# Performance work log

Hardware: AMD Instinct MI355X
Metric: run time of the kernel (lower is better)

## Reference

```python
import jax, jax.numpy as jnp
import numpy as np

NL, NK = 10000, 2000          # ligand / keypoint node counts
ELL, EKL = 320000, 160000     # lig->lig and kp->lig edge counts
IN, HID, OUT = 128, 128, 128  # in_size, hidden_size, out_size
FDIM = 2 * IN + 1             # edge MLP input: [h_src, h_dst, dij]


def silu(x):
    return x * jax.nn.sigmoid(x)


def setup_inputs() -> dict:
    keys = iter(jax.random.split(jax.random.key(0), 64))

    def nrm(shape, scale=0.02):
        return jax.random.normal(next(keys), shape, dtype=jnp.float32) * scale

    d = {}
    d["h_lig"] = jax.random.normal(next(keys), (NL, IN), dtype=jnp.float32)
    d["h_kp"] = jax.random.normal(next(keys), (NK, IN), dtype=jnp.float32)
    d["x_lig"] = jax.random.normal(next(keys), (NL, 3), dtype=jnp.float32)
    d["x_kp"] = jax.random.normal(next(keys), (NK, 3), dtype=jnp.float32)
    # per-node normalizer (e.g. neighbor count); keep >= 1 to avoid blowup
    d["z_lig"] = jax.random.uniform(next(keys), (NL, 1), dtype=jnp.float32, minval=1.0, maxval=32.0)
    for e in ("ll", "kl"):
        d[e + "_eW1"] = nrm((FDIM, HID)); d[e + "_eb1"] = jnp.zeros((HID,), jnp.float32)
        d[e + "_eW2"] = nrm((HID, HID)); d[e + "_eb2"] = jnp.zeros((HID,), jnp.float32)
        d[e + "_aW"] = nrm((HID, 1)); d[e + "_ab"] = jnp.zeros((1,), jnp.float32)
        d[e + "_cW1"] = nrm((FDIM, HID)); d[e + "_cb1"] = jnp.zeros((HID,), jnp.float32)
        d[e + "_cW2"] = nrm((HID, HID)); d[e + "_cb2"] = jnp.zeros((HID,), jnp.float32)
        d[e + "_cW3"] = nrm((HID, 1), scale=0.001)  # xavier gain=0.001 final coord layer
    d["n_W1"] = nrm((IN + HID, HID)); d["n_b1"] = jnp.zeros((HID,), jnp.float32)
    d["n_W2"] = nrm((HID, OUT)); d["n_b2"] = jnp.zeros((OUT,), jnp.float32)
    d["ll_src"] = jax.random.randint(next(keys), (ELL,), 0, NL, dtype=jnp.int32)
    d["ll_dst"] = jax.random.randint(next(keys), (ELL,), 0, NL, dtype=jnp.int32)
    d["kl_src"] = jax.random.randint(next(keys), (EKL,), 0, NK, dtype=jnp.int32)
    d["kl_dst"] = jax.random.randint(next(keys), (EKL,), 0, NL, dtype=jnp.int32)
    return d


def _edge_messages(hs, hd, xs, xd, eW1, eb1, eW2, eb2, aW, ab, cW1, cb1, cW2, cb2, cW3):
    x_diff = xs - xd                                     # fn.u_sub_v
    dij = jnp.linalg.norm(x_diff, axis=1, keepdims=True)  # [E,1]
    x_diff = x_diff / (dij + 1.0)
    f = jnp.concatenate([hs, hd, dij], axis=1)           # [E, 2*IN+1]
    m = silu(f @ eW1 + eb1)
    m = silu(m @ eW2 + eb2)
    msg_h = m * jax.nn.sigmoid(m @ aW + ab)              # soft attention gate
    c = silu(f @ cW1 + cb1)
    c = silu(c @ cW2 + cb2)
    msg_x = (c @ cW3) * x_diff                           # use_tanh=False path
    return msg_h, msg_x


def reference(h_lig, h_kp, x_lig, x_kp, z_lig,
              ll_eW1, ll_eb1, ll_eW2, ll_eb2, ll_aW, ll_ab,
              ll_cW1, ll_cb1, ll_cW2, ll_cb2, ll_cW3,
              kl_eW1, kl_eb1, kl_eW2, kl_eb2, kl_aW, kl_ab,
              kl_cW1, kl_cb1, kl_cW2, kl_cb2, kl_cW3,
              n_W1, n_b1, n_W2, n_b2,
              ll_src, ll_dst, kl_src, kl_dst):
    # lig -> lig edges
    mh_ll, mx_ll = _edge_messages(h_lig[ll_src], h_lig[ll_dst], x_lig[ll_src], x_lig[ll_dst],
                                  ll_eW1, ll_eb1, ll_eW2, ll_eb2, ll_aW, ll_ab,
                                  ll_cW1, ll_cb1, ll_cW2, ll_cb2, ll_cW3)
    # kp -> lig edges
    mh_kl, mx_kl = _edge_messages(h_kp[kl_src], h_lig[kl_dst], x_kp[kl_src], x_lig[kl_dst],
                                  kl_eW1, kl_eb1, kl_eW2, kl_eb2, kl_aW, kl_ab,
                                  kl_cW1, kl_cb1, kl_cW2, kl_cb2, kl_cW3)
    nl = h_lig.shape[0]
    # multi_update_all with cross_reducer='sum', then per-node normalization by z
    h_neigh = (jax.ops.segment_sum(mh_ll, ll_dst, num_segments=nl)
               + jax.ops.segment_sum(mh_kl, kl_dst, num_segments=nl)) / z_lig
    x_neigh = (jax.ops.segment_sum(mx_ll, ll_dst, num_segments=nl)
               + jax.ops.segment_sum(mx_kl, kl_dst, num_segments=nl)) / z_lig
    nin = jnp.concatenate([h_lig, h_neigh], axis=1)
    h_out = h_lig + (silu(nin @ n_W1 + n_b1) @ n_W2 + n_b2)  # norm=False -> Identity
    x_out = x_lig + x_neigh
    return (h_out, x_out)
```

## Files before the change

### kernel.cpp

```cpp
#include <hip/hip_runtime.h>
#include <hip/hip_bf16.h>
#include <math.h>

#define EPB  32
#define MSTR 136
#define FSTR 264

typedef __attribute__((ext_vector_type(8))) short short8;
typedef __attribute__((ext_vector_type(4))) float f32x4;

__device__ __forceinline__ unsigned short f2bf(float x) {
    unsigned int u = __float_as_uint(x);
    u += 0x7fffu + ((u >> 16) & 1u);
    return (unsigned short)(u >> 16);
}
__device__ __forceinline__ float bf2f(short v) {
    return __uint_as_float(((unsigned int)(unsigned short)v) << 16);
}
__device__ __forceinline__ unsigned int pkbf(float a, float b) {
    __hip_bfloat162 h = __float22bfloat162_rn(make_float2(a, b));
    union { __hip_bfloat162 h2; unsigned int u; } cv; cv.h2 = h; return cv.u;
}
__device__ __forceinline__ float frcp(float x) { return __builtin_amdgcn_rcpf(x); }
__device__ __forceinline__ float fsilu(float x) {
    return x * frcp(1.0f + __expf(-x));
}
__device__ __forceinline__ float fsigm(float x) {
    return frcp(1.0f + __expf(-x));
}
__device__ __forceinline__ void atomAddF(float* p, float v) {
    unsafeAtomicAdd(p, v);
}

template<int CTRL>
__device__ __forceinline__ float dppAdd(float x) {
    int y = __builtin_amdgcn_update_dpp(0, __float_as_int(x), CTRL, 0xF, 0xF, false);
    return x + __int_as_float(y);
}
__device__ __forceinline__ float rowSum16(float g) {
    g = dppAdd<0xB1>(g);
    g = dppAdd<0x4E>(g);
    g = dppAdd<0x124>(g);
    g = dppAdd<0x128>(g);
    return g;
}

struct PrepArgs { const float* src[10]; };

__global__ __launch_bounds__(256) void prep_hist_kernel(PrepArgs pa, short* __restrict__ wsb,
                                                        const int* __restrict__ lld,
                                                        const int* __restrict__ kld,
                                                        int* __restrict__ hist,
                                                        float* __restrict__ zfill) {
    int idx = blockIdx.x * 256 + threadIdx.x;
    if (idx < 245760) {
        int pair = idx / 49152;
        int rem  = idx - pair * 49152;
        int second = (rem >= 32768) ? 1 : 0;
        int mi = pair * 2 + second;
        int within = second ? (rem - 32768) : rem;
        int n, k, K;
        if (second) { K = 128; n = within >> 7; k = within & 127; }
        else        { K = 256; n = within >> 8; k = within & 255; }
        int dstoff = pair * 49152 + second * 32768;
        wsb[dstoff + n * K + k] = (short)f2bf(pa.src[mi][k * 128 + n]);
        return;
    }
    idx -= 245760;
    if (idx < 320000) { atomicAdd(&hist[lld[idx]], 1); return; }
    idx -= 320000;
    if (idx < 160000) { atomicAdd(&hist[10000 + kld[idx]], 1); return; }
    idx -= 160000;
    if (idx < 327500)
        ((float4*)zfill)[idx] = make_float4(0.f, 0.f, 0.f, 0.f);
}

struct ProjPair { const float* A; const short* Bt0; const short* Bt1; short* out;
                  const float* b0; const float* b1; int rows; int ktb; int hasb; };
struct BArgs {
    const int* hist;
    int* cursor;
    ProjPair p[4];
};

__global__ __launch_bounds__(256) void scan_proj_kernel(BArgs ba) {
    __shared__ __align__(16) short a_lds[64 * MSTR];
    const int t = threadIdx.x;
    if (blockIdx.x < 2) {
        __shared__ int ps[256];
        const int* h = ba.hist + blockIdx.x * 10000;
        int* cur = ba.cursor + blockIdx.x * 10000;
        const int base = t * 40;
        int v[40];
#pragma unroll
        for (int i = 0; i < 40; i++) {
            int ii = base + i;
            v[i] = (ii < 10000) ? h[ii] : 0;
        }
        int s = 0;
#pragma unroll
        for (int i = 0; i < 40; i++) s += v[i];
        ps[t] = s;
        __syncthreads();
        for (int off = 1; off < 256; off <<= 1) {
            int x = (t >= off) ? ps[t - off] : 0;
            __syncthreads();
            ps[t] += x;
            __syncthreads();
        }
        int run = ps[t] - s;
#pragma unroll
        for (int i = 0; i < 40; i++) {
            int ii = base + i;
            if (ii < 10000) { cur[ii] = run; run += v[i]; }
        }
        return;
    }
    const int pb = blockIdx.x - 2;
    const int pi = pb / 157, tile = pb - pi * 157;
    const ProjPair pd = ba.p[pi];
    if (tile * 64 >= pd.rows) return;
    {
        const int r = t >> 2, q = t & 3;
        const int node = tile * 64 + r;
        short* arow = a_lds + r * MSTR + q * 32;
        if (node < pd.rows) {
            const float* ap = pd.A + (size_t)node * 128 + q * 32;
#pragma unroll
            for (int i = 0; i < 4; i++) {
                float4 v0 = *(const float4*)(ap + i * 8);
                float4 v1 = *(const float4*)(ap + i * 8 + 4);
                uint4 o;
                o.x = pkbf(v0.x, v0.y); o.y = pkbf(v0.z, v0.w);
                o.z = pkbf(v1.x, v1.y); o.w = pkbf(v1.z, v1.w);
                *(uint4*)(arow + i * 8) = o;
            }
        } else {
            uint4 z = make_uint4(0, 0, 0, 0);
#pragma unroll
            for (int i = 0; i < 4; i++) *(uint4*)(arow + i * 8) = z;
        }
    }
    __syncthreads();

    const int ln = t & 63, wv = t >> 6;
    const int lrow = ln & 15, quad = ln >> 4;
    const int c0 = wv * 32 + lrow, c1 = c0 + 16;

#pragma unroll
    for (int g = 0; g < 2; g++) {
        const short* Bt = g ? pd.Bt1 : pd.Bt0;
        const float* bias = g ? pd.b1 : pd.b0;
        const int co = g * 128;
        short8 bf0[4], bf1[4];
#pragma unroll
        for (int kt = 0; kt < 4; kt++) {
            bf0[kt] = *(const short8*)(Bt + c0 * 256 + (pd.ktb + kt) * 32 + quad * 8);
            bf1[kt] = *(const short8*)(Bt + c1 * 256 + (pd.ktb + kt) * 32 + quad * 8);
        }
        const float bb0 = pd.hasb ? bias[c0] : 0.0f;
        const float bb1 = pd.hasb ? bias[c1] : 0.0f;
#pragma unroll
        for (int mt = 0; mt < 4; mt++) {
            short8 af[4];
#pragma unroll
            for (int kt = 0; kt < 4; kt++)
                af[kt] = *(const short8*)(&a_lds[(mt * 16 + lrow) * MSTR + kt * 32 + quad * 8]);
            f32x4 a0 = {0.f, 0.f, 0.f, 0.f}, a1 = {0.f, 0.f, 0.f, 0.f};
#pragma unroll
            for (int kt = 0; kt < 4; kt++) {
                a0 = __builtin_amdgcn_mfma_f32_16x16x32_bf16(af[kt], bf0[kt], a0, 0, 0, 0);
                a1 = __builtin_amdgcn_mfma_f32_16x16x32_bf16(af[kt], bf1[kt], a1, 0, 0, 0);
            }
#pragma unroll
            for (int r = 0; r < 4; r++) {
                const int node = tile * 64 + mt * 16 + quad * 4 + r;
                if (node < pd.rows) {
                    pd.out[(size_t)node * 256 + co + c0] = (short)f2bf(a0[r] + bb0);
                    pd.out[(size_t)node * 256 + co + c1] = (short)f2bf(a1[r] + bb1);
                }
            }
        }
    }
}

struct SArgs {
    const int *lls, *lld, *kls, *kld;
    int* cursor;
    int2 *ll_spk, *kl_spk;
};

__global__ __launch_bounds__(256) void scatter_kernel(SArgs sa) {
    int i = blockIdx.x * 256 + threadIdx.x;
    if (i < 320000) {
        int s = sa.lls[i];
        int d = sa.lld[i];
        int p = atomicAdd(&sa.cursor[d], 1);
        sa.ll_spk[p] = make_int2(s, d);
    } else if (i < 480000) {
        int j = i - 320000;
        int s = sa.kls[j];
        int d = sa.kld[j];
        int p = atomicAdd(&sa.cursor[10000 + d], 1);
        sa.kl_spk[p] = make_int2(s, d);
    }
}

struct EdgeSet {
    const short *Ps, *Pd;
    const float *xs, *xd;
    const int2 *esd;
    const float *w256e, *w256c;
    const short *W2t, *cW2t;
    const float *b2e, *b2c;
    const float *aW, *ab, *cW3;
};
struct EdgePair { EdgeSet s[2]; int split; };

__global__ __launch_bounds__(256, 6) void edge_kernel(EdgePair ep,
                                                      float* __restrict__ hne,
                                                      float* __restrict__ xne)
{
    __shared__ __align__(16) char mbuf[EPB * MSTR * 4];
    __shared__ float sv_l[EPB];
    __shared__ float gate_l[EPB];
    __shared__ float xdf[3][EPB];
    __shared__ int   dstl[EPB];
    __shared__ float gpc[4][EPB];
    __shared__ float gpe[4][EPB];

    short* mh = (short*)mbuf;
    short* mc = (short*)(mbuf + EPB * MSTR * 2);
    float* msg = (float*)mbuf;

    const int isKL = (blockIdx.x >= ep.split) ? 1 : 0;
    const EdgeSet P = ep.s[isKL];
    int b = blockIdx.x - (isKL ? ep.split : 0);
    const int nb8 = isKL ? 625 : 1250;
    b = (b & 7) * nb8 + (b >> 3);
    const int eb = b * EPB;
    const int t = threadIdx.x;

    {
        const int e = t >> 3, q = t & 7;
        const int eid = eb + e;
        const int2 sd = P.esd[eid];
        const int s = sd.x, d = sd.y;
        const short* psrow = P.Ps + (size_t)s * 256 + q * 16;
        const short* pdrow = P.Pd + (size_t)d * 256 + q * 16;
        short8 ra[2][2], rb[2][2];
#pragma unroll
        for (int path = 0; path < 2; path++)
#pragma unroll
            for (int i = 0; i < 2; i++) {
                ra[path][i] = *(const short8*)(psrow + path * 128 + i * 8);
                rb[path][i] = *(const short8*)(pdrow + path * 128 + i * 8);
            }
        float dx = P.xs[s * 3 + 0] - P.xd[d * 3 + 0];
        float dy = P.xs[s * 3 + 1] - P.xd[d * 3 + 1];
        float dz = P.xs[s * 3 + 2] - P.xd[d * 3 + 2];
        float dd = __builtin_amdgcn_sqrtf(dx * dx + dy * dy + dz * dz);
        if (q == 0) {
            dstl[e] = d;
            float inv = frcp(dd + 1.0f);
            xdf[0][e] = dx * inv; xdf[1][e] = dy * inv; xdf[2][e] = dz * inv;
        }
#pragma unroll
        for (int path = 0; path < 2; path++) {
            const float* wq = (path ? P.w256c : P.w256e) + q * 16;
            short* mrow = (path ? mc : mh) + e * MSTR + q * 16;
#pragma unroll
            for (int i = 0; i < 2; i++) {
                short8 a = ra[path][i];
                short8 b2 = rb[path][i];
                float4 wA = *(const float4*)(wq + i * 8);
                float4 wB = *(const float4*)(wq + i * 8 + 4);
                float v0 = fsilu(bf2f(a[0]) + bf2f(b2[0]) + dd * wA.x);
                float v1 = fsilu(bf2f(a[1]) + bf2f(b2[1]) + dd * wA.y);
                float v2 = fsilu(bf2f(a[2]) + bf2f(b2[2]) + dd * wA.z);
                float v3 = fsilu(bf2f(a[3]) + bf2f(b2[3]) + dd * wA.w);
                float v4 = fsilu(bf2f(a[4]) + bf2f(b2[4]) + dd * wB.x);
                float v5 = fsilu(bf2f(a[5]) + bf2f(b2[5]) + dd * wB.y);
                float v6 = fsilu(bf2f(a[6]) + bf2f(b2[6]) + dd * wB.z);
                float v7 = fsilu(bf2f(a[7]) + bf2f(b2[7]) + dd * wB.w);
                uint4 o;
                o.x = pkbf(v0, v1); o.y = pkbf(v2, v3);
                o.z = pkbf(v4, v5); o.w = pkbf(v6, v7);
                *(uint4*)(mrow + i * 8) = o;
            }
        }
    }
    __syncthreads();

    const int ln = t & 63, wv = t >> 6;
    const int lrow = ln & 15, quad = ln >> 4;
    const int c0 = wv * 32 + lrow, c1 = c0 + 16;

    {
        short8 bf0[4], bf1[4];
#pragma unroll
        for (int kt = 0; kt < 4; kt++) {
            bf0[kt] = *(const short8*)(P.cW2t + c0 * 128 + kt * 32 + quad * 8);
            bf1[kt] = *(const short8*)(P.cW2t + c1 * 128 + kt * 32 + quad * 8);
        }
        const float cw0 = P.cW3[c0], cw1 = P.cW3[c1];
        const float bb0 = P.b2c[c0], bb1 = P.b2c[c1];
#pragma unroll
        for (int mt = 0; mt < 2; mt++) {
            short8 af[4];
#pragma unroll
            for (int kt = 0; kt < 4; kt++)
                af[kt] = *(const short8*)(&mc[(mt * 16 + lrow) * MSTR + kt * 32 + quad * 8]);
            f32x4 a0 = {0.f, 0.f, 0.f, 0.f}, a1 = {0.f, 0.f, 0.f, 0.f};
#pragma unroll
            for (int kt = 0; kt < 4; kt++) {
                a0 = __builtin_amdgcn_mfma_f32_16x16x32_bf16(af[kt], bf0[kt], a0, 0, 0, 0);
                a1 = __builtin_amdgcn_mfma_f32_16x16x32_bf16(af[kt], bf1[kt], a1, 0, 0, 0);
            }
#pragma unroll
            for (int r = 0; r < 4; r++) {
                float v0 = fsilu(a0[r] + bb0);
                float v1 = fsilu(a1[r] + bb1);
                float g = rowSum16(v0 * cw0 + v1 * cw1);
                if (lrow == 0) gpc[wv][mt * 16 + quad * 4 + r] = g;
            }
        }
    }

    float m2s[2][8];
    {
        short8 bf0[4], bf1[4];
#pragma unroll
        for (int kt = 0; kt < 4; kt++) {
            bf0[kt] = *(const short8*)(P.W2t + c0 * 128 + kt * 32 + quad * 8);
            bf1[kt] = *(const short8*)(P.W2t + c1 * 128 + kt * 32 + quad * 8);
        }
        const float aw0 = P.aW[c0], aw1 = P.aW[c1];
        const float bb0 = P.b2e[c0], bb1 = P.b2e[c1];
#pragma unroll
        for (int mt = 0; mt < 2; mt++) {
            short8 af[4];
#pragma unroll
            for (int kt = 0; kt < 4; kt++)
                af[kt] = *(const short8*)(&mh[(mt * 16 + lrow) * MSTR + kt * 32 + quad * 8]);
            f32x4 a0 = {0.f, 0.f, 0.f, 0.f}, a1 = {0.f, 0.f, 0.f, 0.f};
#pragma unroll
            for (int kt = 0; kt < 4; kt++) {
                a0 = __builtin_amdgcn_mfma_f32_16x16x32_bf16(af[kt], bf0[kt], a0, 0, 0, 0);
                a1 = __builtin_amdgcn_mfma_f32_16x16x32_bf16(af[kt], bf1[kt], a1, 0, 0, 0);
            }
#pragma unroll
            for (int r = 0; r < 4; r++) {
                float v0 = fsilu(a0[r] + bb0);
                float v1 = fsilu(a1[r] + bb1);
                m2s[mt][r] = v0; m2s[mt][4 + r] = v1;
                float g = rowSum16(v0 * aw0 + v1 * aw1);
                if (lrow == 0) gpe[wv][mt * 16 + quad * 4 + r] = g;
            }
        }
    }
    __syncthreads();

    if (t < EPB) {
        sv_l[t]   = gpc[0][t] + gpc[1][t] + gpc[2][t] + gpc[3][t];
        gate_l[t] = fsigm(gpe[0][t] + gpe[1][t] + gpe[2][t] + gpe[3][t] + P.ab[0]);
    }
#pragma unroll
    for (int mt = 0; mt < 2; mt++)
#pragma unroll
        for (int r = 0; r < 4; r++) {
            const int erow = mt * 16 + quad * 4 + r;
            msg[erow * 132 + c0] = m2s[mt][r];
            msg[erow * 132 + c1] = m2s[mt][4 + r];
        }
    __syncthreads();

    {
        const int col = t & 127;
        const int e0 = (t >> 7) * 16;
        float acc = 0.0f;
        int cur = dstl[e0];
#pragma unroll 4
        for (int e = e0; e < e0 + 16; e++) {
            const int d = dstl[e];
            if (d != cur) {
                atomAddF(&hne[(size_t)cur * 128 + col], acc);
                acc = 0.0f; cur = d;
            }
            acc += msg[e * 132 + col] * gate_l[e];
        }
        atomAddF(&hne[(size_t)cur * 128 + col], acc);
    }
    if (t < 6) {
        const int ax = (t >= 3) ? (t - 3) : t;
        const int e0 = (t >= 3) ? 16 : 0;
        float acc = 0.0f;
        int cur = dstl[e0];
        for (int e = e0; e < e0 + 16; e++) {
            const int d = dstl[e];
            if (d != cur) {
                atomAddF(&xne[cur * 3 + ax], acc);
                acc = 0.0f; cur = d;
            }
            acc += sv_l[e] * xdf[ax][e];
        }
        atomAddF(&xne[cur * 3 + ax], acc);
    }
}

__global__ __launch_bounds__(256) void node_kernel(
    const float* __restrict__ h_lig, const float* __restrict__ zlig,
    const short* __restrict__ W1t, const float* __restrict__ b1v,
    const short* __restrict__ W2t, const float* __restrict__ b2v,
    const float* __restrict__ x_lig,
    const float* __restrict__ acc_h, const float* __restrict__ acc_x,
    float* __restrict__ h_out, float* __restrict__ x_out)
{
    __shared__ __align__(16) short f_lds[64 * FSTR];
    __shared__ __align__(16) short m_lds[64 * MSTR];
    const int t = threadIdx.x;
    const int nb = blockIdx.x * 64;

    {
        const int e = t >> 2, q = t & 3;
        const int node = nb + e;
        short* frow = &f_lds[e * FSTR + q * 32];
        if (node < 10000) {
            const float zi = frcp(zlig[node]);
            const float4* hp = (const float4*)(h_lig + (size_t)node * 128 + q * 32);
            const float4* np = (const float4*)(acc_h + (size_t)node * 128 + q * 32);
#pragma unroll
            for (int i = 0; i < 8; i++) {
                float4 v = hp[i];
                *(uint2*)(frow + i * 4) = make_uint2(pkbf(v.x, v.y), pkbf(v.z, v.w));
            }
#pragma unroll
            for (int i = 0; i < 8; i++) {
                float4 v = np[i];
                *(uint2*)(frow + 128 + i * 4) =
                    make_uint2(pkbf(v.x * zi, v.y * zi), pkbf(v.z * zi, v.w * zi));
            }
        } else {
            const uint2 zz = make_uint2(0, 0);
#pragma unroll
            for (int i = 0; i < 8; i++) {
                *(uint2*)(frow + i * 4) = zz;
                *(uint2*)(frow + 128 + i * 4) = zz;
            }
        }
    }
    __syncthreads();

    const int ln = t & 63, wv = t >> 6;
    const int lrow = ln & 15, quad = ln >> 4;
    const int c0 = wv * 32 + lrow, c1 = c0 + 16;

    {
        short8 bf0[8], bf1[8];
#pragma unroll
        for (int kt = 0; kt < 8; kt++) {
            bf0[kt] = *(const short8*)(W1t + c0 * 256 + kt * 32 + quad * 8);
            bf1[kt] = *(const short8*)(W1t + c1 * 256 + kt * 32 + quad * 8);
        }
        const float bb0 = b1v[c0], bb1 = b1v[c1];
#pragma unroll
        for (int mt = 0; mt < 4; mt++) {
            short8 af[8];
#pragma unroll
            for (int kt = 0; kt < 8; kt++)
                af[kt] = *(const short8*)(&f_lds[(mt * 16 + lrow) * FSTR + kt * 32 + quad * 8]);
            f32x4 a0 = {0.f, 0.f, 0.f, 0.f}, a1 = {0.f, 0.f, 0.f, 0.f};
#pragma unroll
            for (int kt = 0; kt < 8; kt++) {
                a0 = __builtin_amdgcn_mfma_f32_16x16x32_bf16(af[kt], bf0[kt], a0, 0, 0, 0);
                a1 = __builtin_amdgcn_mfma_f32_16x16x32_bf16(af[kt], bf1[kt], a1, 0, 0, 0);
            }
#pragma unroll
            for (int r = 0; r < 4; r++) {
                const int erow = mt * 16 + quad * 4 + r;
                m_lds[erow * MSTR + c0] = (short)f2bf(fsilu(a0[r] + bb0));
                m_lds[erow * MSTR + c1] = (short)f2bf(fsilu(a1[r] + bb1));
            }
        }
    }
    __syncthreads();

    {
        short8 bf0[4], bf1[4];
#pragma unroll
        for (int kt = 0; kt < 4; kt++) {
            bf0[kt] = *(const short8*)(W2t + c0 * 128 + kt * 32 + quad * 8);
            bf1[kt] = *(const short8*)(W2t + c1 * 128 + kt * 32 + quad * 8);
        }
        const float bb0 = b2v[c0], bb1 = b2v[c1];
#pragma unroll
        for (int mt = 0; mt < 4; mt++) {
            short8 af[4];
#pragma unroll
            for (int kt = 0; kt < 4; kt++)
                af[kt] = *(const short8*)(&m_lds[(mt * 16 + lrow) * MSTR + kt * 32 + quad * 8]);
            f32x4 a0 = {0.f, 0.f, 0.f, 0.f}, a1 = {0.f, 0.f, 0.f, 0.f};
#pragma unroll
            for (int kt = 0; kt < 4; kt++) {
                a0 = __builtin_amdgcn_mfma_f32_16x16x32_bf16(af[kt], bf0[kt], a0, 0, 0, 0);
                a1 = __builtin_amdgcn_mfma_f32_16x16x32_bf16(af[kt], bf1[kt], a1, 0, 0, 0);
            }
#pragma unroll
            for (int r = 0; r < 4; r++) {
                const int node = nb + mt * 16 + quad * 4 + r;
                if (node < 10000) {
                    h_out[(size_t)node * 128 + c0] = a0[r] + bb0 + h_lig[(size_t)node * 128 + c0];
                    h_out[(size_t)node * 128 + c1] = a1[r] + bb1 + h_lig[(size_t)node * 128 + c1];
                }
            }
        }
    }
    if (t < 64) {
        const int node = nb + t;
        if (node < 10000) {
            const float zi = frcp(zlig[node]);
#pragma unroll
            for (int i = 0; i < 3; i++)
                x_out[node * 3 + i] = x_lig[node * 3 + i] + acc_x[node * 3 + i] * zi;
        }
    }
}

extern "C" void kernel_launch(void* const* d_in, const int* in_sizes, int n_in,
                              void* d_out, int out_size, void* d_ws, size_t ws_size,
                              hipStream_t stream)
{
    (void)in_sizes; (void)n_in; (void)ws_size; (void)out_size;
    const float* h_lig  = (const float*)d_in[0];
    const float* h_kp   = (const float*)d_in[1];
    const float* x_lig  = (const float*)d_in[2];
    const float* x_kp   = (const float*)d_in[3];
    const float* z_lig  = (const float*)d_in[4];
    const float* ll_eW1 = (const float*)d_in[5];
    const float* ll_eb1 = (const float*)d_in[6];
    const float* ll_eW2 = (const float*)d_in[7];
    const float* ll_eb2 = (const float*)d_in[8];
    const float* ll_aW  = (const float*)d_in[9];
    const float* ll_ab  = (const float*)d_in[10];
    const float* ll_cW1 = (const float*)d_in[11];
    const float* ll_cb1 = (const float*)d_in[12];
    const float* ll_cW2 = (const float*)d_in[13];
    const float* ll_cb2 = (const float*)d_in[14];
    const float* ll_cW3 = (const float*)d_in[15];
    const float* kl_eW1 = (const float*)d_in[16];
    const float* kl_eb1 = (const float*)d_in[17];
    const float* kl_eW2 = (const float*)d_in[18];
    const float* kl_eb2 = (const float*)d_in[19];
    const float* kl_aW  = (const float*)d_in[20];
    const float* kl_ab  = (const float*)d_in[21];
    const float* kl_cW1 = (const float*)d_in[22];
    const float* kl_cb1 = (const float*)d_in[23];
    const float* kl_cW2 = (const float*)d_in[24];
    const float* kl_cb2 = (const float*)d_in[25];
    const float* kl_cW3 = (const float*)d_in[26];
    const float* n_W1   = (const float*)d_in[27];
    const float* n_b1   = (const float*)d_in[28];
    const float* n_W2   = (const float*)d_in[29];
    const float* n_b2   = (const float*)d_in[30];
    const int* ll_src = (const int*)d_in[31];
    const int* ll_dst = (const int*)d_in[32];
    const int* kl_src = (const int*)d_in[33];
    const int* kl_dst = (const int*)d_in[34];

    float* h_out = (float*)d_out;
    float* x_out = h_out + 1280000;

    char* wsc = (char*)d_ws;
    short* wsb    = (short*)wsc;
    short* P_ll_s = (short*)(wsc +   491520);
    short* P_ll_d = (short*)(wsc +  5611520);
    short* P_kl_s = (short*)(wsc + 10731520);
    short* P_kl_d = (short*)(wsc + 11755520);
    int2* ll_spk  = (int2*)(wsc + 16875520);
    int2* kl_spk  = (int2*)(wsc + 19435520);
    int* hist     = (int*)(wsc + 20715520);
    int* cursor   = (int*)(wsc + 20795520);
    float* hne    = (float*)(wsc + 20875520);
    float* xne    = (float*)(wsc + 25995520);

    (void)hipMemsetAsync(hist, 0, 80000, stream);

    {
        PrepArgs pa;
        pa.src[0] = ll_eW1; pa.src[1] = ll_eW2; pa.src[2] = ll_cW1; pa.src[3] = ll_cW2;
        pa.src[4] = kl_eW1; pa.src[5] = kl_eW2; pa.src[6] = kl_cW1; pa.src[7] = kl_cW2;
        pa.src[8] = n_W1;   pa.src[9] = n_W2;
        prep_hist_kernel<<<4115, 256, 0, stream>>>(pa, wsb, ll_dst, kl_dst, hist, hne);
    }
    {
        BArgs ba;
        ba.hist = hist; ba.cursor = cursor;
        ba.p[0] = { h_lig, wsb + 0,     wsb + 49152,  P_ll_s, ll_eb1, ll_cb1, 10000, 0, 0 };
        ba.p[1] = { h_lig, wsb + 0,     wsb + 49152,  P_ll_d, ll_eb1, ll_cb1, 10000, 4, 1 };
        ba.p[2] = { h_kp,  wsb + 98304, wsb + 147456, P_kl_s, kl_eb1, kl_cb1,  2000, 0, 0 };
        ba.p[3] = { h_lig, wsb + 98304, wsb + 147456, P_kl_d, kl_eb1, kl_cb1, 10000, 4, 1 };
        scan_proj_kernel<<<2 + 4 * 157, 256, 0, stream>>>(ba);
    }
    {
        SArgs sa;
        sa.lls = ll_src; sa.lld = ll_dst; sa.kls = kl_src; sa.kld = kl_dst;
        sa.cursor = cursor;
        sa.ll_spk = ll_spk; sa.kl_spk = kl_spk;
        scatter_kernel<<<1875, 256, 0, stream>>>(sa);
    }
    {
        EdgePair ep;
        ep.split = 10000;
        ep.s[0] = { P_ll_s, P_ll_d, x_lig, x_lig, ll_spk,
                    ll_eW1 + 256 * 128, ll_cW1 + 256 * 128,
                    wsb + 32768, wsb + 81920, ll_eb2, ll_cb2,
                    ll_aW, ll_ab, ll_cW3 };
        ep.s[1] = { P_kl_s, P_kl_d, x_kp, x_lig, kl_spk,
                    kl_eW1 + 256 * 128, kl_cW1 + 256 * 128,
                    wsb + 131072, wsb + 180224, kl_eb2, kl_cb2,
                    kl_aW, kl_ab, kl_cW3 };
        edge_kernel<<<15000, 256, 0, stream>>>(ep, hne, xne);
    }
    node_kernel<<<157, 256, 0, stream>>>(
        h_lig, z_lig, wsb + 196608, n_b1, wsb + 229376, n_b2,
        x_lig, hne, xne, h_out, x_out);
}
```

Measured before the change: 371.0 us.

## Process four edge tiles per block with double-buffered gather prefetch; fuse scatter with projection

The edge kernel now handles four 32-edge tiles per block. It prefetches the next tile's gathered projections into registers and double-buffers the LDS message tiles, so gather latency overlaps the MFMA work of the current tile. The grid shrinks from 15000 to 3750 blocks, and occupancy drops from 6 to 4 blocks per CU because LDS use roughly doubles. Separately, the scan is split into its own tiny kernel and the scatter is fused into the projection kernel. The weight-transpose loop in prep is also reindexed so its reads are coalesced.

Measured after the change: 400.1 us. 1.08x slower.

```diff
diff --git a/kernel.cpp b/kernel.cpp
--- a/kernel.cpp
+++ b/kernel.cpp
@@ -2,9 +2,10 @@
 #include <hip/hip_bf16.h>
 #include <math.h>
 
-#define EPB  32
-#define MSTR 136
-#define FSTR 264
+#define EPB   32
+#define TEDGE 4
+#define MSTR  136
+#define FSTR  264
 
 typedef __attribute__((ext_vector_type(8))) short short8;
 typedef __attribute__((ext_vector_type(4))) float f32x4;
@@ -59,9 +60,9 @@
         int second = (rem >= 32768) ? 1 : 0;
         int mi = pair * 2 + second;
         int within = second ? (rem - 32768) : rem;
-        int n, k, K;
-        if (second) { K = 128; n = within >> 7; k = within & 127; }
-        else        { K = 256; n = within >> 8; k = within & 255; }
+        int K = second ? 128 : 256;
+        int n = within & 127;
+        int k = within >> 7;
         int dstoff = pair * 49152 + second * 32768;
         wsb[dstoff + n * K + k] = (short)f2bf(pa.src[mi][k * 128 + n]);
         return;
@@ -75,50 +76,69 @@
         ((float4*)zfill)[idx] = make_float4(0.f, 0.f, 0.f, 0.f);
 }
 
+__global__ __launch_bounds__(256) void scan_kernel(const int* __restrict__ hist,
+                                                   int* __restrict__ cursor) {
+    __shared__ int ps[256];
+    const int t = threadIdx.x;
+    const int* h = hist + blockIdx.x * 10000;
+    int* cur = cursor + blockIdx.x * 10000;
+    const int base = t * 40;
+    int v[40];
+#pragma unroll
+    for (int i = 0; i < 40; i++) {
+        int ii = base + i;
+        v[i] = (ii < 10000) ? h[ii] : 0;
+    }
+    int s = 0;
+#pragma unroll
+    for (int i = 0; i < 40; i++) s += v[i];
+    ps[t] = s;
+    __syncthreads();
+    for (int off = 1; off < 256; off <<= 1) {
+        int x = (t >= off) ? ps[t - off] : 0;
+        __syncthreads();
+        ps[t] += x;
+        __syncthreads();
+    }
+    int run = ps[t] - s;
+#pragma unroll
+    for (int i = 0; i < 40; i++) {
+        int ii = base + i;
+        if (ii < 10000) { cur[ii] = run; run += v[i]; }
+    }
+}
+
 struct ProjPair { const float* A; const short* Bt0; const short* Bt1; short* out;
                   const float* b0; const float* b1; int rows; int ktb; int hasb; };
-struct BArgs {
-    const int* hist;
+struct CArgs {
+    const int *lls, *lld, *kls, *kld;
     int* cursor;
+    int2 *ll_spk, *kl_spk;
     ProjPair p[4];
 };
 
-__global__ __launch_bounds__(256) void scan_proj_kernel(BArgs ba) {
+__global__ __launch_bounds__(256) void scatter_proj_kernel(CArgs ca) {
     __shared__ __align__(16) short a_lds[64 * MSTR];
     const int t = threadIdx.x;
-    if (blockIdx.x < 2) {
-        __shared__ int ps[256];
-        const int* h = ba.hist + blockIdx.x * 10000;
-        int* cur = ba.cursor + blockIdx.x * 10000;
-        const int base = t * 40;
-        int v[40];
-#pragma unroll
-        for (int i = 0; i < 40; i++) {
-            int ii = base + i;
-            v[i] = (ii < 10000) ? h[ii] : 0;
-        }
-        int s = 0;
-#pragma unroll
-        for (int i = 0; i < 40; i++) s += v[i];
-        ps[t] = s;
-        __syncthreads();
-        for (int off = 1; off < 256; off <<= 1) {
-            int x = (t >= off) ? ps[t - off] : 0;
-            __syncthreads();
-            ps[t] += x;
-            __syncthreads();
-        }
-        int run = ps[t] - s;
-#pragma unroll
-        for (int i = 0; i < 40; i++) {
-            int ii = base + i;
-            if (ii < 10000) { cur[ii] = run; run += v[i]; }
+    if (blockIdx.x < 1875) {
+        int i = blockIdx.x * 256 + t;
+        if (i < 320000) {
+            int s = ca.lls[i];
+            int d = ca.lld[i];
+            int p = atomicAdd(&ca.cursor[d], 1);
+            ca.ll_spk[p] = make_int2(s, d);
+        } else if (i < 480000) {
+            int j = i - 320000;
+            int s = ca.kls[j];
+            int d = ca.kld[j];
+            int p = atomicAdd(&ca.cursor[10000 + d], 1);
+            ca.kl_spk[p] = make_int2(s, d);
         }
         return;
     }
-    const int pb = blockIdx.x - 2;
+    const int pb = blockIdx.x - 1875;
     const int pi = pb / 157, tile = pb - pi * 157;
-    const ProjPair pd = ba.p[pi];
+    const ProjPair pd = ca.p[pi];
     if (tile * 64 >= pd.rows) return;
     {
         const int r = t >> 2, q = t & 3;
@@ -181,28 +201,6 @@
                 }
             }
         }
-    }
-}
-
-struct SArgs {
-    const int *lls, *lld, *kls, *kld;
-    int* cursor;
-    int2 *ll_spk, *kl_spk;
-};
-
-__global__ __launch_bounds__(256) void scatter_kernel(SArgs sa) {
-    int i = blockIdx.x * 256 + threadIdx.x;
-    if (i < 320000) {
-        int s = sa.lls[i];
-        int d = sa.lld[i];
-        int p = atomicAdd(&sa.cursor[d], 1);
-        sa.ll_spk[p] = make_int2(s, d);
-    } else if (i < 480000) {
-        int j = i - 320000;
-        int s = sa.kls[j];
-        int d = sa.kld[j];
-        int p = atomicAdd(&sa.cursor[10000 + d], 1);
-        sa.kl_spk[p] = make_int2(s, d);
     }
 }
 
@@ -215,40 +213,53 @@
     const float *b2e, *b2c;
     const float *aW, *ab, *cW3;
 };
-struct EdgePair { EdgeSet s[2]; int split; };
-
-__global__ __launch_bounds__(256, 6) void edge_kernel(EdgePair ep,
+struct EdgePair { EdgeSet s[2]; };
+
+__global__ __launch_bounds__(256, 4) void edge_kernel(EdgePair ep,
                                                       float* __restrict__ hne,
                                                       float* __restrict__ xne)
 {
-    __shared__ __align__(16) char mbuf[EPB * MSTR * 4];
+    __shared__ __align__(16) char mbuf[2][EPB * MSTR * 4];
     __shared__ float sv_l[EPB];
     __shared__ float gate_l[EPB];
-    __shared__ float xdf[3][EPB];
-    __shared__ int   dstl[EPB];
+    __shared__ float xdf[2][3][EPB];
+    __shared__ int   dstl[2][EPB];
     __shared__ float gpc[4][EPB];
     __shared__ float gpe[4][EPB];
 
-    short* mh = (short*)mbuf;
-    short* mc = (short*)(mbuf + EPB * MSTR * 2);
-    float* msg = (float*)mbuf;
-
-    const int isKL = (blockIdx.x >= ep.split) ? 1 : 0;
+    const int isKL = (blockIdx.x >= 2500) ? 1 : 0;
     const EdgeSet P = ep.s[isKL];
-    int b = blockIdx.x - (isKL ? ep.split : 0);
-    const int nb8 = isKL ? 625 : 1250;
-    b = (b & 7) * nb8 + (b >> 3);
-    const int eb = b * EPB;
+    int b = blockIdx.x - (isKL ? 2500 : 0);
+    {
+        const int nb = isKL ? 1250 : 2500;
+        const int q8 = nb >> 3, r8 = nb & 7;
+        const int xcd = b & 7, bi = b >> 3;
+        b = (xcd < r8 ? xcd * (q8 + 1) : r8 * (q8 + 1) + (xcd - r8) * q8) + bi;
+    }
+    const int tile0 = b * TEDGE;
     const int t = threadIdx.x;
-
-    {
-        const int e = t >> 3, q = t & 7;
-        const int eid = eb + e;
+    const int e = t >> 3, q = t & 7;
+    const int ln = t & 63, wv = t >> 6;
+    const int lrow = ln & 15, quad = ln >> 4;
+    const int c0 = wv * 32 + lrow, c1 = c0 + 16;
+
+    const float cw3_0 = P.cW3[c0], cw3_1 = P.cW3[c1];
+    const float b2c_0 = P.b2c[c0], b2c_1 = P.b2c[c1];
+    const float aw_0  = P.aW[c0],  aw_1  = P.aW[c1];
+    const float b2e_0 = P.b2e[c0], b2e_1 = P.b2e[c1];
+    const float ab0   = P.ab[0];
+
+    short8 ra[2][2], rb[2][2];
+    float sdx, sdy, sdz, sdd;
+    int   sd_d;
+
+    auto STAGE = [&](int g) {
+        const int eid = g * EPB + e;
         const int2 sd = P.esd[eid];
         const int s = sd.x, d = sd.y;
+        sd_d = d;
         const short* psrow = P.Ps + (size_t)s * 256 + q * 16;
         const short* pdrow = P.Pd + (size_t)d * 256 + q * 16;
-        short8 ra[2][2], rb[2][2];
 #pragma unroll
         for (int path = 0; path < 2; path++)
 #pragma unroll
@@ -256,22 +267,28 @@
                 ra[path][i] = *(const short8*)(psrow + path * 128 + i * 8);
                 rb[path][i] = *(const short8*)(pdrow + path * 128 + i * 8);
             }
-        float dx = P.xs[s * 3 + 0] - P.xd[d * 3 + 0];
-        float dy = P.xs[s * 3 + 1] - P.xd[d * 3 + 1];
-        float dz = P.xs[s * 3 + 2] - P.xd[d * 3 + 2];
-        float dd = __builtin_amdgcn_sqrtf(dx * dx + dy * dy + dz * dz);
+        sdx = P.xs[s * 3 + 0] - P.xd[d * 3 + 0];
+        sdy = P.xs[s * 3 + 1] - P.xd[d * 3 + 1];
+        sdz = P.xs[s * 3 + 2] - P.xd[d * 3 + 2];
+        sdd = __builtin_amdgcn_sqrtf(sdx * sdx + sdy * sdy + sdz * sdz);
+    };
+
+    auto PACK = [&](int nx) {
+        short* mhw = (short*)mbuf[nx];
+        short* mcw = mhw + EPB * MSTR;
         if (q == 0) {
-            dstl[e] = d;
-            float inv = frcp(dd + 1.0f);
-            xdf[0][e] = dx * inv; xdf[1][e] = dy * inv; xdf[2][e] = dz * inv;
-        }
+            dstl[nx][e] = sd_d;
+            float inv = frcp(sdd + 1.0f);
+            xdf[nx][0][e] = sdx * inv; xdf[nx][1][e] = sdy * inv; xdf[nx][2][e] = sdz * inv;
+        }
+        const float dd = sdd;
 #pragma unroll
         for (int path = 0; path < 2; path++) {
             const float* wq = (path ? P.w256c : P.w256e) + q * 16;
-            short* mrow = (path ? mc : mh) + e * MSTR + q * 16;
+            short* mrow = (path ? mcw : mhw) + e * MSTR + q * 16;
 #pragma unroll
             for (int i = 0; i < 2; i++) {
-                short8 a = ra[path][i];
+                short8 a  = ra[path][i];
                 short8 b2 = rb[path][i];
                 float4 wA = *(const float4*)(wq + i * 8);
                 float4 wB = *(const float4*)(wq + i * 8 + 4);
@@ -289,122 +306,127 @@
                 *(uint4*)(mrow + i * 8) = o;
             }
         }
-    }
+    };
+
+    STAGE(tile0);
+    PACK(0);
     __syncthreads();
 
-    const int ln = t & 63, wv = t >> 6;
-    const int lrow = ln & 15, quad = ln >> 4;
-    const int c0 = wv * 32 + lrow, c1 = c0 + 16;
-
-    {
-        short8 bf0[4], bf1[4];
-#pragma unroll
-        for (int kt = 0; kt < 4; kt++) {
-            bf0[kt] = *(const short8*)(P.cW2t + c0 * 128 + kt * 32 + quad * 8);
-            bf1[kt] = *(const short8*)(P.cW2t + c1 * 128 + kt * 32 + quad * 8);
-        }
-        const float cw0 = P.cW3[c0], cw1 = P.cW3[c1];
-        const float bb0 = P.b2c[c0], bb1 = P.b2c[c1];
-#pragma unroll
-        for (int mt = 0; mt < 2; mt++) {
-            short8 af[4];
-#pragma unroll
-            for (int kt = 0; kt < 4; kt++)
-                af[kt] = *(const short8*)(&mc[(mt * 16 + lrow) * MSTR + kt * 32 + quad * 8]);
-            f32x4 a0 = {0.f, 0.f, 0.f, 0.f}, a1 = {0.f, 0.f, 0.f, 0.f};
+    for (int ti = 0; ti < TEDGE; ++ti) {
+        const int cur = ti & 1;
+        short* mh  = (short*)mbuf[cur];
+        short* mc  = mh + EPB * MSTR;
+        float* msg = (float*)mbuf[cur];
+
+        if (ti + 1 < TEDGE) STAGE(tile0 + ti + 1);
+
+        {
+            short8 bf0[4], bf1[4];
 #pragma unroll
             for (int kt = 0; kt < 4; kt++) {
-                a0 = __builtin_amdgcn_mfma_f32_16x16x32_bf16(af[kt], bf0[kt], a0, 0, 0, 0);
-                a1 = __builtin_amdgcn_mfma_f32_16x16x32_bf16(af[kt], bf1[kt], a1, 0, 0, 0);
-            }
+                bf0[kt] = *(const short8*)(P.cW2t + c0 * 128 + kt * 32 + quad * 8);
+                bf1[kt] = *(const short8*)(P.cW2t + c1 * 128 + kt * 32 + quad * 8);
+            }
+#pragma unroll
+            for (int mt = 0; mt < 2; mt++) {
+                short8 af[4];
+#pragma unroll
+                for (int kt = 0; kt < 4; kt++)
+                    af[kt] = *(const short8*)(&mc[(mt * 16 + lrow) * MSTR + kt * 32 + quad * 8]);
+                f32x4 a0 = {0.f, 0.f, 0.f, 0.f}, a1 = {0.f, 0.f, 0.f, 0.f};
+#pragma unroll
+                for (int kt = 0; kt < 4; kt++) {
+                    a0 = __builtin_amdgcn_mfma_f32_16x16x32_bf16(af[kt], bf0[kt], a0, 0, 0, 0);
+                    a1 = __builtin_amdgcn_mfma_f32_16x16x32_bf16(af[kt], bf1[kt], a1, 0, 0, 0);
+                }
+#pragma unroll
+                for (int r = 0; r < 4; r++) {
+                    float v0 = fsilu(a0[r] + b2c_0);
+                    float v1 = fsilu(a1[r] + b2c_1);
+                    float g = rowSum16(v0 * cw3_0 + v1 * cw3_1);
+                    if (lrow == 0) gpc[wv][mt * 16 + quad * 4 + r] = g;
+                }
+            }
+        }
+
+        float m2s[2][8];
+        {
+            short8 bf0[4], bf1[4];
+#pragma unroll
+            for (int kt = 0; kt < 4; kt++) {
+                bf0[kt] = *(const short8*)(P.W2t + c0 * 128 + kt * 32 + quad * 8);
+                bf1[kt] = *(const short8*)(P.W2t + c1 * 128 + kt * 32 + quad * 8);
+            }
+#pragma unroll
+            for (int mt = 0; mt < 2; mt++) {
+                short8 af[4];
+#pragma unroll
+                for (int kt = 0; kt < 4; kt++)
+                    af[kt] = *(const short8*)(&mh[(mt * 16 + lrow) * MSTR + kt * 32 + quad * 8]);
+                f32x4 a0 = {0.f, 0.f, 0.f, 0.f}, a1 = {0.f, 0.f, 0.f, 0.f};
+#pragma unroll
+                for (int kt = 0; kt < 4; kt++) {
+                    a0 = __builtin_amdgcn_mfma_f32_16x16x32_bf16(af[kt], bf0[kt], a0, 0, 0, 0);
+                    a1 = __builtin_amdgcn_mfma_f32_16x16x32_bf16(af[kt], bf1[kt], a1, 0, 0, 0);
+                }
+#pragma unroll
+                for (int r = 0; r < 4; r++) {
+                    float v0 = fsilu(a0[r] + b2e_0);
+                    float v1 = fsilu(a1[r] + b2e_1);
+                    m2s[mt][r] = v0; m2s[mt][4 + r] = v1;
+                    float g = rowSum16(v0 * aw_0 + v1 * aw_1);
+                    if (lrow == 0) gpe[wv][mt * 16 + quad * 4 + r] = g;
+                }
+            }
+        }
+        __syncthreads();
+
+        if (t < EPB) {
+            sv_l[t]   = gpc[0][t] + gpc[1][t] + gpc[2][t] + gpc[3][t];
+            gate_l[t] = fsigm(gpe[0][t] + gpe[1][t] + gpe[2][t] + gpe[3][t] + ab0);
+        }
+#pragma unroll
+        for (int mt = 0; mt < 2; mt++)
 #pragma unroll
             for (int r = 0; r < 4; r++) {
-                float v0 = fsilu(a0[r] + bb0);
-                float v1 = fsilu(a1[r] + bb1);
-                float g = rowSum16(v0 * cw0 + v1 * cw1);
-                if (lrow == 0) gpc[wv][mt * 16 + quad * 4 + r] = g;
-            }
-        }
-    }
-
-    float m2s[2][8];
-    {
-        short8 bf0[4], bf1[4];
-#pragma unroll
-        for (int kt = 0; kt < 4; kt++) {
-            bf0[kt] = *(const short8*)(P.W2t + c0 * 128 + kt * 32 + quad * 8);
-            bf1[kt] = *(const short8*)(P.W2t + c1 * 128 + kt * 32 + quad * 8);
-        }
-        const float aw0 = P.aW[c0], aw1 = P.aW[c1];
-        const float bb0 = P.b2e[c0], bb1 = P.b2e[c1];
-#pragma unroll
-        for (int mt = 0; mt < 2; mt++) {
-            short8 af[4];
-#pragma unroll
-            for (int kt = 0; kt < 4; kt++)
-                af[kt] = *(const short8*)(&mh[(mt * 16 + lrow) * MSTR + kt * 32 + quad * 8]);
-            f32x4 a0 = {0.f, 0.f, 0.f, 0.f}, a1 = {0.f, 0.f, 0.f, 0.f};
-#pragma unroll
-            for (int kt = 0; kt < 4; kt++) {
-                a0 = __builtin_amdgcn_mfma_f32_16x16x32_bf16(af[kt], bf0[kt], a0, 0, 0, 0);
-                a1 = __builtin_amdgcn_mfma_f32_16x16x32_bf16(af[kt], bf1[kt], a1, 0, 0, 0);
-            }
-#pragma unroll
-            for (int r = 0; r < 4; r++) {
-                float v0 = fsilu(a0[r] + bb0);
-                float v1 = fsilu(a1[r] + bb1);
-                m2s[mt][r] = v0; m2s[mt][4 + r] = v1;
-                float g = rowSum16(v0 * aw0 + v1 * aw1);
-                if (lrow == 0) gpe[wv][mt * 16 + quad * 4 + r] = g;
-            }
-        }
-    }
-    __syncthreads();
-
-    if (t < EPB) {
-        sv_l[t]   = gpc[0][t] + gpc[1][t] + gpc[2][t] + gpc[3][t];
-        gate_l[t] = fsigm(gpe[0][t] + gpe[1][t] + gpe[2][t] + gpe[3][t] + P.ab[0]);
-    }
-#pragma unroll
-    for (int mt = 0; mt < 2; mt++)
-#pragma unroll
-        for (int r = 0; r < 4; r++) {
-            const int erow = mt * 16 + quad * 4 + r;
-            msg[erow * 132 + c0] = m2s[mt][r];
-            msg[erow * 132 + c1] = m2s[mt][4 + r];
-        }
-    __syncthreads();
-
-    {
-        const int col = t & 127;
-        const int e0 = (t >> 7) * 16;
-        float acc = 0.0f;
-        int cur = dstl[e0];
+                const int erow = mt * 16 + quad * 4 + r;
+                msg[erow * 132 + c0] = m2s[mt][r];
+                msg[erow * 132 + c1] = m2s[mt][4 + r];
+            }
+        if (ti + 1 < TEDGE) PACK(cur ^ 1);
+        __syncthreads();
+
+        {
+            const int col = t & 127;
+            const int e0 = (t >> 7) * 16;
+            float acc = 0.0f;
+            int curd = dstl[cur][e0];
 #pragma unroll 4
-        for (int e = e0; e < e0 + 16; e++) {
-            const int d = dstl[e];
-            if (d != cur) {
-                atomAddF(&hne[(size_t)cur * 128 + col], acc);
-                acc = 0.0f; cur = d;
-            }
-            acc += msg[e * 132 + col] * gate_l[e];
-        }
-        atomAddF(&hne[(size_t)cur * 128 + col], acc);
-    }
-    if (t < 6) {
-        const int ax = (t >= 3) ? (t - 3) : t;
-        const int e0 = (t >= 3) ? 16 : 0;
-        float acc = 0.0f;
-        int cur = dstl[e0];
-        for (int e = e0; e < e0 + 16; e++) {
-            const int d = dstl[e];
-            if (d != cur) {
-                atomAddF(&xne[cur * 3 + ax], acc);
-                acc = 0.0f; cur = d;
-            }
-            acc += sv_l[e] * xdf[ax][e];
-        }
-        atomAddF(&xne[cur * 3 + ax], acc);
+            for (int ee = e0; ee < e0 + 16; ee++) {
+                const int d = dstl[cur][ee];
+                if (d != curd) {
+                    atomAddF(&hne[(size_t)curd * 128 + col], acc);
+                    acc = 0.0f; curd = d;
+                }
+                acc += msg[ee * 132 + col] * gate_l[ee];
+            }
+            atomAddF(&hne[(size_t)curd * 128 + col], acc);
+        }
+        if (t < 6) {
+            const int ax = (t >= 3) ? (t - 3) : t;
+            const int e0 = (t >= 3) ? 16 : 0;
+            float acc = 0.0f;
+            int curd = dstl[cur][e0];
+            for (int ee = e0; ee < e0 + 16; ee++) {
+                const int d = dstl[cur][ee];
+                if (d != curd) {
+                    atomAddF(&xne[curd * 3 + ax], acc);
+                    acc = 0.0f; curd = d;
+                }
+                acc += sv_l[ee] * xdf[cur][ax][ee];
+            }
+            atomAddF(&xne[curd * 3 + ax], acc);
+        }
     }
 }
 
@@ -592,25 +614,20 @@
         pa.src[8] = n_W1;   pa.src[9] = n_W2;
         prep_hist_kernel<<<4115, 256, 0, stream>>>(pa, wsb, ll_dst, kl_dst, hist, hne);
     }
-    {
-        BArgs ba;
-        ba.hist = hist; ba.cursor = cursor;
-        ba.p[0] = { h_lig, wsb + 0,     wsb + 49152,  P_ll_s, ll_eb1, ll_cb1, 10000, 0, 0 };
-        ba.p[1] = { h_lig, wsb + 0,     wsb + 49152,  P_ll_d, ll_eb1, ll_cb1, 10000, 4, 1 };
-        ba.p[2] = { h_kp,  wsb + 98304, wsb + 147456, P_kl_s, kl_eb1, kl_cb1,  2000, 0, 0 };
-        ba.p[3] = { h_lig, wsb + 98304, wsb + 147456, P_kl_d, kl_eb1, kl_cb1, 10000, 4, 1 };
-        scan_proj_kernel<<<2 + 4 * 157, 256, 0, stream>>>(ba);
-    }
-    {
-        SArgs sa;
-        sa.lls = ll_src; sa.lld = ll_dst; sa.kls = kl_src; sa.kld = kl_dst;
-        sa.cursor = cursor;
-        sa.ll_spk = ll_spk; sa.kl_spk = kl_spk;
-        scatter_kernel<<<1875, 256, 0, stream>>>(sa);
+    scan_kernel<<<2, 256, 0, stream>>>(hist, cursor);
+    {
+        CArgs ca;
+        ca.lls = ll_src; ca.lld = ll_dst; ca.kls = kl_src; ca.kld = kl_dst;
+        ca.cursor = cursor;
+        ca.ll_spk = ll_spk; ca.kl_spk = kl_spk;
+        ca.p[0] = { h_lig, wsb + 0,     wsb + 49152,  P_ll_s, ll_eb1, ll_cb1, 10000, 0, 0 };
+        ca.p[1] = { h_lig, wsb + 0,     wsb + 49152,  P_ll_d, ll_eb1, ll_cb1, 10000, 4, 1 };
+        ca.p[2] = { h_kp,  wsb + 98304, wsb + 147456, P_kl_s, kl_eb1, kl_cb1,  2000, 0, 0 };
+        ca.p[3] = { h_lig, wsb + 98304, wsb + 147456, P_kl_d, kl_eb1, kl_cb1, 10000, 4, 1 };
+        scatter_proj_kernel<<<1875 + 4 * 157, 256, 0, stream>>>(ca);
     }
     {
         EdgePair ep;
-        ep.split = 10000;
         ep.s[0] = { P_ll_s, P_ll_d, x_lig, x_lig, ll_spk,
                     ll_eW1 + 256 * 128, ll_cW1 + 256 * 128,
                     wsb + 32768, wsb + 81920, ll_eb2, ll_cb2,
@@ -619,7 +636,7 @@
                     kl_eW1 + 256 * 128, kl_cW1 + 256 * 128,
                     wsb + 131072, wsb + 180224, kl_eb2, kl_cb2,
                     kl_aW, kl_ab, kl_cW3 };
-        edge_kernel<<<15000, 256, 0, stream>>>(ep, hne, xne);
+        edge_kernel<<<3750, 256, 0, stream>>>(ep, hne, xne);
     }
     node_kernel<<<157, 256, 0, stream>>>(
         h_lig, z_lig, wsb + 196608, n_b1, wsb + 229376, n_b2,
```

## Fuse histogram into scan blocks via LDS bins and merge scatter with projection

Applied to the files above, without the earlier changes.

The dst-degree histogram moves from global atomics into two blocks that count bins in shared memory and then scan them, which removes the hipMemsetAsync and one kernel launch. The weight transpose indexing now makes consecutive threads read contiguous source elements. The edge scatter and the node projection GEMM now share one launch, so the projection no longer waits behind the scatter kernel. The cost is that two single blocks walk 320k and 160k indices serially, which may lengthen the critical path of the prep kernel.

After: 425.9 us. 14.8% more time.

```diff
diff --git a/kernel.cpp b/kernel.cpp
--- a/kernel.cpp
+++ b/kernel.cpp
@@ -47,55 +47,32 @@
 
 struct PrepArgs { const float* src[10]; };
 
-__global__ __launch_bounds__(256) void prep_hist_kernel(PrepArgs pa, short* __restrict__ wsb,
+__global__ __launch_bounds__(256) void prep_scan_kernel(PrepArgs pa, short* __restrict__ wsb,
                                                         const int* __restrict__ lld,
                                                         const int* __restrict__ kld,
-                                                        int* __restrict__ hist,
+                                                        int* __restrict__ cursor,
                                                         float* __restrict__ zfill) {
-    int idx = blockIdx.x * 256 + threadIdx.x;
-    if (idx < 245760) {
-        int pair = idx / 49152;
-        int rem  = idx - pair * 49152;
-        int second = (rem >= 32768) ? 1 : 0;
-        int mi = pair * 2 + second;
-        int within = second ? (rem - 32768) : rem;
-        int n, k, K;
-        if (second) { K = 128; n = within >> 7; k = within & 127; }
-        else        { K = 256; n = within >> 8; k = within & 255; }
-        int dstoff = pair * 49152 + second * 32768;
-        wsb[dstoff + n * K + k] = (short)f2bf(pa.src[mi][k * 128 + n]);
-        return;
-    }
-    idx -= 245760;
-    if (idx < 320000) { atomicAdd(&hist[lld[idx]], 1); return; }
-    idx -= 320000;
-    if (idx < 160000) { atomicAdd(&hist[10000 + kld[idx]], 1); return; }
-    idx -= 160000;
-    if (idx < 327500)
-        ((float4*)zfill)[idx] = make_float4(0.f, 0.f, 0.f, 0.f);
-}
-
-struct ProjPair { const float* A; const short* Bt0; const short* Bt1; short* out;
-                  const float* b0; const float* b1; int rows; int ktb; int hasb; };
-struct BArgs {
-    const int* hist;
-    int* cursor;
-    ProjPair p[4];
-};
-
-__global__ __launch_bounds__(256) void scan_proj_kernel(BArgs ba) {
-    __shared__ __align__(16) short a_lds[64 * MSTR];
+    __shared__ int bins[10000];
+    __shared__ int ps[256];
     const int t = threadIdx.x;
     if (blockIdx.x < 2) {
-        __shared__ int ps[256];
-        const int* h = ba.hist + blockIdx.x * 10000;
-        int* cur = ba.cursor + blockIdx.x * 10000;
+        const int n4 = blockIdx.x ? 40000 : 80000;
+        const int4* d4 = (const int4*)(blockIdx.x ? kld : lld);
+        int* cur = cursor + blockIdx.x * 10000;
+        for (int i = t; i < 10000; i += 256) bins[i] = 0;
+        __syncthreads();
+        for (int i = t; i < n4; i += 256) {
+            int4 v = d4[i];
+            atomicAdd(&bins[v.x], 1); atomicAdd(&bins[v.y], 1);
+            atomicAdd(&bins[v.z], 1); atomicAdd(&bins[v.w], 1);
+        }
+        __syncthreads();
         const int base = t * 40;
         int v[40];
 #pragma unroll
         for (int i = 0; i < 40; i++) {
             int ii = base + i;
-            v[i] = (ii < 10000) ? h[ii] : 0;
+            v[i] = (ii < 10000) ? bins[ii] : 0;
         }
         int s = 0;
 #pragma unroll
@@ -116,9 +93,56 @@
         }
         return;
     }
-    const int pb = blockIdx.x - 2;
+    int idx = (blockIdx.x - 2) * 256 + t;
+    if (idx < 245760) {
+        int pair = idx / 49152;
+        int rem  = idx - pair * 49152;
+        int second = (rem >= 32768) ? 1 : 0;
+        int mi = pair * 2 + second;
+        int within = second ? (rem - 32768) : rem;
+        int K = second ? 128 : 256;
+        int n = within & 127;
+        int k = within >> 7;
+        int dstoff = pair * 49152 + second * 32768;
+        wsb[dstoff + n * K + k] = (short)f2bf(pa.src[mi][k * 128 + n]);
+        return;
+    }
+    idx -= 245760;
+    if (idx < 327500)
+        ((float4*)zfill)[idx] = make_float4(0.f, 0.f, 0.f, 0.f);
+}
+
+struct ProjPair { const float* A; const short* Bt0; const short* Bt1; short* out;
+                  const float* b0; const float* b1; int rows; int ktb; int hasb; };
+struct CArgs {
+    const int *lls, *lld, *kls, *kld;
+    int* cursor;
+    int2 *ll_spk, *kl_spk;
+    ProjPair p[4];
+};
+
+__global__ __launch_bounds__(256) void scatter_proj_kernel(CArgs ca) {
+    __shared__ __align__(16) short a_lds[64 * MSTR];
+    const int t = threadIdx.x;
+    if (blockIdx.x < 1875) {
+        int i = blockIdx.x * 256 + t;
+        if (i < 320000) {
+            int s = ca.lls[i];
+            int d = ca.lld[i];
+            int p = atomicAdd(&ca.cursor[d], 1);
+            ca.ll_spk[p] = make_int2(s, d);
+        } else if (i < 480000) {
+            int j = i - 320000;
+            int s = ca.kls[j];
+            int d = ca.kld[j];
+            int p = atomicAdd(&ca.cursor[10000 + d], 1);
+            ca.kl_spk[p] = make_int2(s, d);
+        }
+        return;
+    }
+    const int pb = blockIdx.x - 1875;
     const int pi = pb / 157, tile = pb - pi * 157;
-    const ProjPair pd = ba.p[pi];
+    const ProjPair pd = ca.p[pi];
     if (tile * 64 >= pd.rows) return;
     {
         const int r = t >> 2, q = t & 3;
@@ -181,28 +205,6 @@
                 }
             }
         }
-    }
-}
-
-struct SArgs {
-    const int *lls, *lld, *kls, *kld;
-    int* cursor;
-    int2 *ll_spk, *kl_spk;
-};
-
-__global__ __launch_bounds__(256) void scatter_kernel(SArgs sa) {
-    int i = blockIdx.x * 256 + threadIdx.x;
-    if (i < 320000) {
-        int s = sa.lls[i];
-        int d = sa.lld[i];
-        int p = atomicAdd(&sa.cursor[d], 1);
-        sa.ll_spk[p] = make_int2(s, d);
-    } else if (i < 480000) {
-        int j = i - 320000;
-        int s = sa.kls[j];
-        int d = sa.kld[j];
-        int p = atomicAdd(&sa.cursor[10000 + d], 1);
-        sa.kl_spk[p] = make_int2(s, d);
     }
 }
 
@@ -578,35 +580,27 @@
     short* P_kl_d = (short*)(wsc + 11755520);
     int2* ll_spk  = (int2*)(wsc + 16875520);
     int2* kl_spk  = (int2*)(wsc + 19435520);
-    int* hist     = (int*)(wsc + 20715520);
     int* cursor   = (int*)(wsc + 20795520);
     float* hne    = (float*)(wsc + 20875520);
     float* xne    = (float*)(wsc + 25995520);
-
-    (void)hipMemsetAsync(hist, 0, 80000, stream);
 
     {
         PrepArgs pa;
         pa.src[0] = ll_eW1; pa.src[1] = ll_eW2; pa.src[2] = ll_cW1; pa.src[3] = ll_cW2;
         pa.src[4] = kl_eW1; pa.src[5] = kl_eW2; pa.src[6] = kl_cW1; pa.src[7] = kl_cW2;
         pa.src[8] = n_W1;   pa.src[9] = n_W2;
-        prep_hist_kernel<<<4115, 256, 0, stream>>>(pa, wsb, ll_dst, kl_dst, hist, hne);
-    }
-    {
-        BArgs ba;
-        ba.hist = hist; ba.cursor = cursor;
-        ba.p[0] = { h_lig, wsb + 0,     wsb + 49152,  P_ll_s, ll_eb1, ll_cb1, 10000, 0, 0 };
-        ba.p[1] = { h_lig, wsb + 0,     wsb + 49152,  P_ll_d, ll_eb1, ll_cb1, 10000, 4, 1 };
-        ba.p[2] = { h_kp,  wsb + 98304, wsb + 147456, P_kl_s, kl_eb1, kl_cb1,  2000, 0, 0 };
-        ba.p[3] = { h_lig, wsb + 98304, wsb + 147456, P_kl_d, kl_eb1, kl_cb1, 10000, 4, 1 };
-        scan_proj_kernel<<<2 + 4 * 157, 256, 0, stream>>>(ba);
-    }
-    {
-        SArgs sa;
-        sa.lls = ll_src; sa.lld = ll_dst; sa.kls = kl_src; sa.kld = kl_dst;
-        sa.cursor = cursor;
-        sa.ll_spk = ll_spk; sa.kl_spk = kl_spk;
-        scatter_kernel<<<1875, 256, 0, stream>>>(sa);
+        prep_scan_kernel<<<2242, 256, 0, stream>>>(pa, wsb, ll_dst, kl_dst, cursor, hne);
+    }
+    {
+        CArgs ca;
+        ca.lls = ll_src; ca.lld = ll_dst; ca.kls = kl_src; ca.kld = kl_dst;
+        ca.cursor = cursor;
+        ca.ll_spk = ll_spk; ca.kl_spk = kl_spk;
+        ca.p[0] = { h_lig, wsb + 0,     wsb + 49152,  P_ll_s, ll_eb1, ll_cb1, 10000, 0, 0 };
+        ca.p[1] = { h_lig, wsb + 0,     wsb + 49152,  P_ll_d, ll_eb1, ll_cb1, 10000, 4, 1 };
+        ca.p[2] = { h_kp,  wsb + 98304, wsb + 147456, P_kl_s, kl_eb1, kl_cb1,  2000, 0, 0 };
+        ca.p[3] = { h_lig, wsb + 98304, wsb + 147456, P_kl_d, kl_eb1, kl_cb1, 10000, 4, 1 };
+        scatter_proj_kernel<<<1875 + 4 * 157, 256, 0, stream>>>(ca);
     }
     {
         EdgePair ep;
```
